# Performance work log

Hardware: AMD Instinct MI355X
Metric: run time of the kernel (lower is better)

The kernel has to match this reference:

```python
import jax, jax.numpy as jnp
import numpy as np

B, C, K, F = 16, 64, 128, 6
HORIZON_S = 3.0  # conflict_horizon_s default
EPS = 1e-06


def setup_inputs() -> dict:
    rng = np.random.default_rng(0)
    # base adjacency: sparse random directed graph, zero diagonal
    A = (rng.random((B, K, K)) < 0.05).astype(np.float32)
    A[:, np.arange(K), np.arange(K)] = 0.0
    # candidates: exactly one unordered-pair edit (state in {0:none,1:i->j,2:j->i})
    cand = np.repeat(A[:, None], C, axis=1).copy()
    i = rng.integers(0, K - 1, (B, C))
    j = i + 1 + (rng.integers(0, K - 1, (B, C)) % (K - 1 - i))
    state = rng.integers(0, 3, (B, C))
    bidx = np.arange(B)[:, None] * np.ones((1, C), dtype=np.int64)
    cidx = np.ones((B, 1), dtype=np.int64) * np.arange(C)[None, :]
    cand[bidx, cidx, i, j] = (state == 1).astype(np.float32)
    cand[bidx, cidx, j, i] = (state == 2).astype(np.float32)
    cand[:, 0] = A  # candidate 0 is NOOP (keep A_t)
    # agent features: (x, y, yaw, vx, vy, pad)
    feat = rng.normal(size=(B, K, F)).astype(np.float32)
    feat[..., 0:2] *= 20.0  # spread positions over ~40m
    mask = (rng.random((B, K)) > 0.1).astype(np.float32)
    return {
        "A_t": jnp.asarray(A),
        "candidate_A": jnp.asarray(cand),
        "agent_feat": jnp.asarray(feat),
        "agent_mask": jnp.asarray(mask),
    }


def _edit_tokens(A_t, candidate_A):
    # vectorized version of EBSTM.extract_edit_tokens
    Bn, Cn, Kn, _ = candidate_A.shape
    base = A_t > 0.5                      # [B,K,K]
    cb = candidate_A > 0.5                # [B,C,K,K]
    diff = cb != base[:, None]            # [B,C,K,K]
    upper = jnp.triu(jnp.ones((Kn, Kn), dtype=bool), k=1)
    pairdiff = (diff | jnp.swapaxes(diff, -1, -2)) & upper
    flat = pairdiff.reshape(Bn, Cn, Kn * Kn)
    changed = flat.any(-1)                # [B,C]
    idx = jnp.argmax(flat, axis=-1)       # first changed pair in row-major (i,j) order
    i = idx // Kn
    j = idx % Kn
    barange = jnp.arange(Bn)[:, None]
    carange = jnp.arange(Cn)[None, :]
    b_ij = base[barange, i, j]
    b_ji = base[barange, j, i]
    c_ij = cb[barange, carange, i, j]
    c_ji = cb[barange, carange, j, i]
    prev = jnp.where(b_ij & ~b_ji, 1, jnp.where(b_ji & ~b_ij, 2, 0))
    nxt = jnp.where(c_ij & ~c_ji, 1, jnp.where(c_ji & ~c_ij, 2, 0))
    tokens = jnp.stack([i, j, prev, nxt], axis=-1).astype(jnp.int32)
    return tokens * changed[..., None].astype(jnp.int32)


def _relation_state3(cb):
    # cb: bool [B,C,K,K]
    at = jnp.swapaxes(cb, -1, -2)
    return ((cb & ~at).astype(jnp.int32) * 1
            + (~cb & at).astype(jnp.int32) * 2
            + (cb & at).astype(jnp.int32) * 3)


def _batched_acyclic(cb, agent_mask):
    # vectorized Kahn zero-indegree peel, matching EBSTM._is_acyclic semantics:
    #  - indegree counts edges from ALL sources (valid or not)
    #  - only valid nodes are ever removed
    #  - special case: <=1 valid node is acyclic
    Bn, Cn, Kn, _ = cb.shape
    valid = (agent_mask > 0.5)[:, None, :]           # [B,1,K]
    Ai = cb.astype(jnp.int32)                        # [B,C,K,K]
    indeg = Ai.sum(axis=-2) * valid.astype(jnp.int32)  # [B,C,K]
    removed = jnp.zeros((Bn, Cn, Kn), dtype=bool)

    def body(t, carry):
        indeg, removed = carry
        rem = valid & (~removed) & (indeg == 0)
        dec = jnp.einsum('bci,bcij->bcj', rem.astype(jnp.int32), Ai)
        return indeg - dec, removed | rem

    indeg, removed = jax.lax.fori_loop(0, Kn, body, (indeg, removed))
    vcount = valid.astype(jnp.int32).sum(-1)          # [B,1]
    return (removed.astype(jnp.int32).sum(-1) == vcount) | (vcount <= 1)


def _pair_dists(agent_feat):
    pos = agent_feat[..., 0:2]
    vel = agent_feat[..., 3:5]
    # _pair_distance: d[b,i,j] = |pos_i - pos_j|
    d = jnp.linalg.norm(pos[:, :, None] - pos[:, None, :], axis=-1)
    # _pair_closest_approach_distance: r[b,i,j] = pos_j - pos_i
    r = pos[:, None, :] - pos[:, :, None]
    v = vel[:, None, :] - vel[:, :, None]
    vv = (v * v).sum(-1)
    rv = (r * v).sum(-1)
    t_star = jnp.clip(-rv / (vv + EPS), 0.0, HORIZON_S)
    dmin = jnp.linalg.norm(r + v * t_star[..., None], axis=-1)
    eye = jnp.eye(dmin.shape[-1], dtype=bool)[None]
    dmin = jnp.where(eye, jnp.inf, dmin)
    return jnp.stack([d, dmin], axis=0)  # [2,B,K,K]


def reference(A_t, candidate_A, agent_feat, agent_mask):
    cb = candidate_A > 0.5
    tokens = _edit_tokens(A_t, candidate_A)          # [B,C,4] int32
    rel = _relation_state3(cb)                       # [B,C,K,K] int32
    acyclic = _batched_acyclic(cb, agent_mask)       # [B,C] bool
    dists = _pair_dists(agent_feat)                  # [2,B,K,K] float32
    return tokens, rel, acyclic, dists
```

## Files before the change

### kernel.cpp

```cpp
#include <hip/hip_runtime.h>
#include <cstdint>
#include <math.h>

#define KN 128
#define BATCH 16
#define CAND 64

typedef float vfloat4 __attribute__((ext_vector_type(4)));

static constexpr size_t TOK_OFF = 0;
static constexpr size_t REL_OFF = (size_t)BATCH * CAND * 4;
static constexpr size_t ACY_OFF = REL_OFF + (size_t)BATCH * CAND * KN * KN;
static constexpr size_t DST_OFF = ACY_OFF + (size_t)BATCH * CAND;

#define DIAG_BIG 1.0e30f

__global__ __launch_bounds__(256) void prep_kernel(const float* __restrict__ A_t,
                                                   const float* __restrict__ feat,
                                                   uint32_t* __restrict__ bits,
                                                   float* __restrict__ out) {
    int t = threadIdx.x;
    {
        int tid  = blockIdx.x * 256 + t;
        int wave = tid >> 6;
        int lane = tid & 63;
        int half = wave & 1;
        int row  = wave >> 1;
        float v = A_t[(size_t)row * KN + half * 64 + lane];
        unsigned long long m = __ballot(v > 0.5f);
        if (lane == 0) {
            bits[row * 4 + half * 2]     = (uint32_t)m;
            bits[row * 4 + half * 2 + 1] = (uint32_t)(m >> 32);
        }
    }
    {
        int bi = 2 * blockIdx.x + (t >> 7);
        int b2 = bi >> 7, i = bi & 127, j = t & 127;
        const float* fi = feat + (size_t)bi * 6;
        const float* fj = feat + (size_t)(b2 * KN + j) * 6;
        float pix = fi[0], piy = fi[1], vix = fi[3], viy = fi[4];
        float pjx = fj[0], pjy = fj[1], vjx = fj[3], vjy = fj[4];
        float dx = pix - pjx, dy = piy - pjy;
        float d = sqrtf(dx * dx + dy * dy);
        float rx = pjx - pix, ry = pjy - piy;
        float vx = vjx - vix, vy = vjy - viy;
        float vv = vx * vx + vy * vy;
        float rv = rx * vx + ry * vy;
        float ts = fminf(fmaxf(-rv / (vv + 1e-6f), 0.0f), 3.0f);
        float mx = rx + vx * ts, my = ry + vy * ts;
        float dmin = (i == j) ? DIAG_BIG : sqrtf(mx * mx + my * my);
        float* o = out + DST_OFF;
        __builtin_nontemporal_store(d,    o + (size_t)(b2 * KN + i) * KN + j);
        __builtin_nontemporal_store(dmin, o + (size_t)((BATCH + b2) * KN + i) * KN + j);
    }
}

__global__ __launch_bounds__(256) void main_kernel(const float* __restrict__ cand,
                                                   const float* __restrict__ mask,
                                                   const uint32_t* __restrict__ baseBits,
                                                   float* __restrict__ out) {
    __shared__ uint32_t adj[KN][5];
    __shared__ uint32_t adjT[KN][6];
    __shared__ uint32_t baseB[KN][4];
    __shared__ uint32_t validW[4];
    __shared__ uint32_t remW2[2][4];
    __shared__ uint32_t removedW[4];
    __shared__ int      minIdx;

    const int t    = threadIdx.x;
    const int lane = t & 63;
    const int wave = t >> 6;
    const int bc   = blockIdx.x;
    const int b    = bc >> 6;

    const float* cptr = cand + (size_t)bc * (KN * KN);
    float* relp = out + REL_OFF + (size_t)bc * (KN * KN);

    float4 c[16];
    const int sub = lane & 31;
    #pragma unroll
    for (int m = 0; m < 16; ++m) {
        int r = (m * 4 + wave) * 2 + (lane >> 5);
        c[m] = ((const float4*)(cptr + (size_t)r * KN))[sub];
    }

    if (t == 0) minIdx = 0x7fffffff;
    if (t < 4)  removedW[t] = 0;

    for (int w = t; w < 512; w += 256) {
        baseB[w >> 2][w & 3] = baseBits[b * 512 + w];
    }

    if (wave < 2) {
        float mv = mask[b * KN + wave * 64 + lane];
        unsigned long long m = __ballot(mv > 0.5f);
        if (lane == 0) {
            validW[wave * 2]     = (uint32_t)m;
            validW[wave * 2 + 1] = (uint32_t)(m >> 32);
        }
    }

    #pragma unroll
    for (int m = 0; m < 16; ++m) {
        int r = (m * 4 + wave) * 2 + (lane >> 5);
        const float4 v = c[m];
        uint32_t nib = (v.x > 0.5f ? 1u : 0u) | (v.y > 0.5f ? 2u : 0u) |
                       (v.z > 0.5f ? 4u : 0u) | (v.w > 0.5f ? 8u : 0u);
        uint32_t word = nib << (4 * (sub & 7));
        word |= __shfl_xor(word, 1);
        word |= __shfl_xor(word, 2);
        word |= __shfl_xor(word, 4);
        if ((lane & 7) == 0) adj[r][sub >> 3] = word;
    }
    __syncthreads();

    {
        const int h = wave >> 1, q = wave & 1;
        uint32_t lo = adj[h * 64 + lane][q * 2];
        uint32_t hi = adj[h * 64 + lane][q * 2 + 1];
        unsigned long long x = ((unsigned long long)hi << 32) | lo;
        const unsigned long long Lm[6] = {
            0x5555555555555555ull, 0x3333333333333333ull, 0x0F0F0F0F0F0F0F0Full,
            0x00FF00FF00FF00FFull, 0x0000FFFF0000FFFFull, 0x00000000FFFFFFFFull };
        #pragma unroll
        for (int k = 0; k < 6; ++k) {
            const int d = 1 << k;
            const unsigned long long L = Lm[k];
            unsigned long long y = __shfl_xor((unsigned long long)x, d);
            x = (lane & d) ? ((x & ~L) | ((y & ~L) >> d))
                           : ((x & L)  | ((y & L) << d));
        }
        adjT[q * 64 + lane][2 * h]     = (uint32_t)x;
        adjT[q * 64 + lane][2 * h + 1] = (uint32_t)(x >> 32);
    }
    __syncthreads();

    uint32_t cT0 = 0, cT1 = 0, cT2 = 0, cT3 = 0;
    int  indeg = 0;
    bool validT = false;
    if (t < KN) {
        cT0 = adjT[t][0]; cT1 = adjT[t][1]; cT2 = adjT[t][2]; cT3 = adjT[t][3];
        validT = (validW[t >> 5] >> (t & 31)) & 1u;
        indeg = validT ? (__popc(cT0) + __popc(cT1) + __popc(cT2) + __popc(cT3)) : 0;
    }

    auto rel_expand = [&]() {
        #pragma unroll
        for (int m = 0; m < 16; ++m) {
            int q  = t + 256 * m;
            int i  = q >> 5;
            int j0 = (q & 31) * 4;
            int iw = j0 >> 5, sh = j0 & 31;
            uint32_t wij = adj[i][iw];
            uint32_t wti = adjT[i][iw];
            uint32_t a4 = (wij >> sh) & 0xFu;
            uint32_t b4 = (wti >> sh) & 0xFu;
            uint32_t packed = ((a4 * 0x00204081u) & 0x01010101u)
                            | (((b4 * 0x00204081u) & 0x01010101u) << 1);
            vfloat4 o;
            o.x = (float)(uint8_t)(packed);
            o.y = (float)(uint8_t)(packed >> 8);
            o.z = (float)(uint8_t)(packed >> 16);
            o.w = (float)(uint8_t)(packed >> 24);
            __builtin_nontemporal_store(o, ((vfloat4*)relp) + q);
        }
    };

    auto logic_phase = [&]() {
        for (int idx = t; idx < 512; idx += 256) {
            int i = idx >> 2, k = idx & 3;
            uint32_t diff = adj[i][k] ^ baseB[i][k];
            if (diff) {
                int base = k * 32;
                uint32_t up, low;
                if (i < base)            { up = diff; low = 0u; }
                else if (i >= base + 31) { up = 0u; low = (i > base + 31) ? diff : (diff & 0x7fffffffu); }
                else {
                    int s = i - base;
                    up  = diff & (0xffffffffu << (s + 1));
                    low = diff & ((1u << s) - 1u);
                }
                int c1 = 0x7fffffff, c2 = 0x7fffffff;
                if (up)  c1 = (i << 7) | (base + __builtin_ctz(up));
                if (low) { int cc2 = base + __builtin_ctz(low); c2 = (cc2 << 7) | i; }
                int cm = min(c1, c2);
                if (cm != 0x7fffffff) atomicMin(&minIdx, cm);
            }
        }
        __syncthreads();

        if (t == 0) {
            float* tok = out + TOK_OFF + (size_t)bc * 4;
            int mi = minIdx;
            if (mi != 0x7fffffff) {
                int i = mi >> 7, j = mi & 127;
                uint32_t b_ij = (baseB[i][j >> 5] >> (j & 31)) & 1u;
                uint32_t b_ji = (baseB[j][i >> 5] >> (i & 31)) & 1u;
                uint32_t c_ij = (adj[i][j >> 5] >> (j & 31)) & 1u;
                uint32_t c_ji = (adj[j][i >> 5] >> (i & 31)) & 1u;
                int prev = (b_ij && !b_ji) ? 1 : ((b_ji && !b_ij) ? 2 : 0);
                int nxt  = (c_ij && !c_ji) ? 1 : ((c_ji && !c_ij) ? 2 : 0);
                tok[0] = (float)i; tok[1] = (float)j; tok[2] = (float)prev; tok[3] = (float)nxt;
            } else {
                tok[0] = 0.f; tok[1] = 0.f; tok[2] = 0.f; tok[3] = 0.f;
            }
        }

        bool removed = false;
        for (int it = 0; it < KN; ++it) {
            const int bsel = it & 1;
            bool rem = (t < KN) && validT && !removed && (indeg == 0);
            unsigned long long m = __ballot(rem);
            if (wave < 2 && lane == 0) {
                remW2[bsel][wave * 2]     = (uint32_t)m;
                remW2[bsel][wave * 2 + 1] = (uint32_t)(m >> 32);
            }
            __syncthreads();
            uint32_t r0 = remW2[bsel][0], r1 = remW2[bsel][1];
            uint32_t r2 = remW2[bsel][2], r3 = remW2[bsel][3];
            if ((r0 | r1 | r2 | r3) == 0u) break;
            if (t < 4) removedW[t] |= remW2[bsel][t];
            if (t < KN) {
                indeg -= __popc(r0 & cT0) + __popc(r1 & cT1) +
                         __popc(r2 & cT2) + __popc(r3 & cT3);
                removed = removed || rem;
            }
        }
        __syncthreads();

        if (t == 0) {
            int rc = __popc(removedW[0]) + __popc(removedW[1]) + __popc(removedW[2]) + __popc(removedW[3]);
            int vc = __popc(validW[0]) + __popc(validW[1]) + __popc(validW[2]) + __popc(validW[3]);
            out[ACY_OFF + bc] = ((rc == vc) || (vc <= 1)) ? 1.0f : 0.0f;
        }
    };

    if (((bc >> 8) & 1) == 0) {
        rel_expand();
        logic_phase();
    } else {
        logic_phase();
        rel_expand();
    }
}

extern "C" void kernel_launch(void* const* d_in, const int* in_sizes, int n_in,
                              void* d_out, int out_size, void* d_ws, size_t ws_size,
                              hipStream_t stream) {
    const float* A_t  = (const float*)d_in[0];
    const float* cand = (const float*)d_in[1];
    const float* feat = (const float*)d_in[2];
    const float* mask = (const float*)d_in[3];
    float* out = (float*)d_out;
    uint32_t* bits = (uint32_t*)d_ws;

    prep_kernel<<<1024, 256, 0, stream>>>(A_t, feat, bits, out);
    main_kernel<<<BATCH * CAND, 256, 0, stream>>>(cand, mask, bits, out);
}
```

Baseline: 123.4 us.

## Split relation expansion into a separate kernel reading packed bit planes

The fused main kernel is split in two. A pack kernel reads the candidates, builds the adjacency and transpose bitsets, writes them to workspace, and computes the tokens and the acyclicity check. A separate rel kernel then expands those bit planes into the large float relation output. The aim is to separate the latency-bound Kahn loop from the bandwidth-bound relation stores so each kernel runs as a uniform phase. The cost is an extra launch and a workspace round-trip of 4 KB per candidate, and the two phases no longer overlap within one block.

Result: slower. 131.1 us (+6.2%).

```diff
diff --git a/kernel.cpp b/kernel.cpp
--- a/kernel.cpp
+++ b/kernel.cpp
@@ -14,6 +14,9 @@
 static constexpr size_t DST_OFF = ACY_OFF + (size_t)BATCH * CAND;
 
 #define DIAG_BIG 1.0e30f
+
+static constexpr size_t WS_BITS  = 0;
+static constexpr size_t WS_PLANE = 2048;
 
 __global__ __launch_bounds__(256) void prep_kernel(const float* __restrict__ A_t,
                                                    const float* __restrict__ feat,
@@ -55,9 +58,10 @@
     }
 }
 
-__global__ __launch_bounds__(256) void main_kernel(const float* __restrict__ cand,
+__global__ __launch_bounds__(256) void pack_kernel(const float* __restrict__ cand,
                                                    const float* __restrict__ mask,
                                                    const uint32_t* __restrict__ baseBits,
+                                                   uint32_t* __restrict__ planes,
                                                    float* __restrict__ out) {
     __shared__ uint32_t adj[KN][5];
     __shared__ uint32_t adjT[KN][6];
@@ -74,7 +78,6 @@
     const int b    = bc >> 6;
 
     const float* cptr = cand + (size_t)bc * (KN * KN);
-    float* relp = out + REL_OFF + (size_t)bc * (KN * KN);
 
     float4 c[16];
     const int sub = lane & 31;
@@ -135,6 +138,55 @@
     }
     __syncthreads();
 
+    {
+        uint32_t* pb = planes + (size_t)bc * 1024;
+        #pragma unroll
+        for (int rep = 0; rep < 2; ++rep) {
+            int w = t + rep * 256;
+            pb[w]       = adj[w >> 2][w & 3];
+            pb[512 + w] = adjT[w >> 2][w & 3];
+        }
+    }
+
+    for (int idx = t; idx < 512; idx += 256) {
+        int i = idx >> 2, k = idx & 3;
+        uint32_t diff = adj[i][k] ^ baseB[i][k];
+        if (diff) {
+            int base = k * 32;
+            uint32_t up, low;
+            if (i < base)            { up = diff; low = 0u; }
+            else if (i >= base + 31) { up = 0u; low = (i > base + 31) ? diff : (diff & 0x7fffffffu); }
+            else {
+                int s = i - base;
+                up  = diff & (0xffffffffu << (s + 1));
+                low = diff & ((1u << s) - 1u);
+            }
+            int c1 = 0x7fffffff, c2 = 0x7fffffff;
+            if (up)  c1 = (i << 7) | (base + __builtin_ctz(up));
+            if (low) { int cc2 = base + __builtin_ctz(low); c2 = (cc2 << 7) | i; }
+            int cm = min(c1, c2);
+            if (cm != 0x7fffffff) atomicMin(&minIdx, cm);
+        }
+    }
+    __syncthreads();
+
+    if (t == 0) {
+        float* tok = out + TOK_OFF + (size_t)bc * 4;
+        int mi = minIdx;
+        if (mi != 0x7fffffff) {
+            int i = mi >> 7, j = mi & 127;
+            uint32_t b_ij = (baseB[i][j >> 5] >> (j & 31)) & 1u;
+            uint32_t b_ji = (baseB[j][i >> 5] >> (i & 31)) & 1u;
+            uint32_t c_ij = (adj[i][j >> 5] >> (j & 31)) & 1u;
+            uint32_t c_ji = (adj[j][i >> 5] >> (i & 31)) & 1u;
+            int prev = (b_ij && !b_ji) ? 1 : ((b_ji && !b_ij) ? 2 : 0);
+            int nxt  = (c_ij && !c_ji) ? 1 : ((c_ji && !c_ij) ? 2 : 0);
+            tok[0] = (float)i; tok[1] = (float)j; tok[2] = (float)prev; tok[3] = (float)nxt;
+        } else {
+            tok[0] = 0.f; tok[1] = 0.f; tok[2] = 0.f; tok[3] = 0.f;
+        }
+    }
+
     uint32_t cT0 = 0, cT1 = 0, cT2 = 0, cT3 = 0;
     int  indeg = 0;
     bool validT = false;
@@ -144,103 +196,65 @@
         indeg = validT ? (__popc(cT0) + __popc(cT1) + __popc(cT2) + __popc(cT3)) : 0;
     }
 
-    auto rel_expand = [&]() {
-        #pragma unroll
-        for (int m = 0; m < 16; ++m) {
-            int q  = t + 256 * m;
-            int i  = q >> 5;
-            int j0 = (q & 31) * 4;
-            int iw = j0 >> 5, sh = j0 & 31;
-            uint32_t wij = adj[i][iw];
-            uint32_t wti = adjT[i][iw];
-            uint32_t a4 = (wij >> sh) & 0xFu;
-            uint32_t b4 = (wti >> sh) & 0xFu;
-            uint32_t packed = ((a4 * 0x00204081u) & 0x01010101u)
-                            | (((b4 * 0x00204081u) & 0x01010101u) << 1);
-            vfloat4 o;
-            o.x = (float)(uint8_t)(packed);
-            o.y = (float)(uint8_t)(packed >> 8);
-            o.z = (float)(uint8_t)(packed >> 16);
-            o.w = (float)(uint8_t)(packed >> 24);
-            __builtin_nontemporal_store(o, ((vfloat4*)relp) + q);
-        }
-    };
-
-    auto logic_phase = [&]() {
-        for (int idx = t; idx < 512; idx += 256) {
-            int i = idx >> 2, k = idx & 3;
-            uint32_t diff = adj[i][k] ^ baseB[i][k];
-            if (diff) {
-                int base = k * 32;
-                uint32_t up, low;
-                if (i < base)            { up = diff; low = 0u; }
-                else if (i >= base + 31) { up = 0u; low = (i > base + 31) ? diff : (diff & 0x7fffffffu); }
-                else {
-                    int s = i - base;
-                    up  = diff & (0xffffffffu << (s + 1));
-                    low = diff & ((1u << s) - 1u);
-                }
-                int c1 = 0x7fffffff, c2 = 0x7fffffff;
-                if (up)  c1 = (i << 7) | (base + __builtin_ctz(up));
-                if (low) { int cc2 = base + __builtin_ctz(low); c2 = (cc2 << 7) | i; }
-                int cm = min(c1, c2);
-                if (cm != 0x7fffffff) atomicMin(&minIdx, cm);
-            }
+    bool removed = false;
+    for (int it = 0; it < KN; ++it) {
+        const int bsel = it & 1;
+        bool rem = (t < KN) && validT && !removed && (indeg == 0);
+        unsigned long long m = __ballot(rem);
+        if (wave < 2 && lane == 0) {
+            remW2[bsel][wave * 2]     = (uint32_t)m;
+            remW2[bsel][wave * 2 + 1] = (uint32_t)(m >> 32);
         }
         __syncthreads();
-
-        if (t == 0) {
-            float* tok = out + TOK_OFF + (size_t)bc * 4;
-            int mi = minIdx;
-            if (mi != 0x7fffffff) {
-                int i = mi >> 7, j = mi & 127;
-                uint32_t b_ij = (baseB[i][j >> 5] >> (j & 31)) & 1u;
-                uint32_t b_ji = (baseB[j][i >> 5] >> (i & 31)) & 1u;
-                uint32_t c_ij = (adj[i][j >> 5] >> (j & 31)) & 1u;
-                uint32_t c_ji = (adj[j][i >> 5] >> (i & 31)) & 1u;
-                int prev = (b_ij && !b_ji) ? 1 : ((b_ji && !b_ij) ? 2 : 0);
-                int nxt  = (c_ij && !c_ji) ? 1 : ((c_ji && !c_ij) ? 2 : 0);
-                tok[0] = (float)i; tok[1] = (float)j; tok[2] = (float)prev; tok[3] = (float)nxt;
-            } else {
-                tok[0] = 0.f; tok[1] = 0.f; tok[2] = 0.f; tok[3] = 0.f;
-            }
-        }
-
-        bool removed = false;
-        for (int it = 0; it < KN; ++it) {
-            const int bsel = it & 1;
-            bool rem = (t < KN) && validT && !removed && (indeg == 0);
-            unsigned long long m = __ballot(rem);
-            if (wave < 2 && lane == 0) {
-                remW2[bsel][wave * 2]     = (uint32_t)m;
-                remW2[bsel][wave * 2 + 1] = (uint32_t)(m >> 32);
-            }
-            __syncthreads();
-            uint32_t r0 = remW2[bsel][0], r1 = remW2[bsel][1];
-            uint32_t r2 = remW2[bsel][2], r3 = remW2[bsel][3];
-            if ((r0 | r1 | r2 | r3) == 0u) break;
-            if (t < 4) removedW[t] |= remW2[bsel][t];
-            if (t < KN) {
-                indeg -= __popc(r0 & cT0) + __popc(r1 & cT1) +
-                         __popc(r2 & cT2) + __popc(r3 & cT3);
-                removed = removed || rem;
-            }
-        }
-        __syncthreads();
-
-        if (t == 0) {
-            int rc = __popc(removedW[0]) + __popc(removedW[1]) + __popc(removedW[2]) + __popc(removedW[3]);
-            int vc = __popc(validW[0]) + __popc(validW[1]) + __popc(validW[2]) + __popc(validW[3]);
-            out[ACY_OFF + bc] = ((rc == vc) || (vc <= 1)) ? 1.0f : 0.0f;
-        }
-    };
-
-    if (((bc >> 8) & 1) == 0) {
-        rel_expand();
-        logic_phase();
-    } else {
-        logic_phase();
-        rel_expand();
+        uint32_t r0 = remW2[bsel][0], r1 = remW2[bsel][1];
+        uint32_t r2 = remW2[bsel][2], r3 = remW2[bsel][3];
+        if ((r0 | r1 | r2 | r3) == 0u) break;
+        if (t < 4) removedW[t] |= remW2[bsel][t];
+        if (t < KN) {
+            indeg -= __popc(r0 & cT0) + __popc(r1 & cT1) +
+                     __popc(r2 & cT2) + __popc(r3 & cT3);
+            removed = removed || rem;
+        }
+    }
+    __syncthreads();
+
+    if (t == 0) {
+        int rc = __popc(removedW[0]) + __popc(removedW[1]) + __popc(removedW[2]) + __popc(removedW[3]);
+        int vc = __popc(validW[0]) + __popc(validW[1]) + __popc(validW[2]) + __popc(validW[3]);
+        out[ACY_OFF + bc] = ((rc == vc) || (vc <= 1)) ? 1.0f : 0.0f;
+    }
+}
+
+__global__ __launch_bounds__(256) void rel_kernel(const uint32_t* __restrict__ planes,
+                                                  float* __restrict__ out) {
+    __shared__ uint32_t plane[1024];
+
+    const int t  = threadIdx.x;
+    const int bc = blockIdx.x;
+
+    uint4 v = ((const uint4*)(planes + (size_t)bc * 1024))[t];
+    ((uint4*)plane)[t] = v;
+    __syncthreads();
+
+    float* relp = out + REL_OFF + (size_t)bc * (KN * KN);
+    #pragma unroll
+    for (int m = 0; m < 16; ++m) {
+        int q  = t + 256 * m;
+        int i  = q >> 5;
+        int j0 = (q & 31) * 4;
+        int iw = j0 >> 5, sh = j0 & 31;
+        uint32_t wij = plane[i * 4 + iw];
+        uint32_t wti = plane[512 + i * 4 + iw];
+        uint32_t a4 = (wij >> sh) & 0xFu;
+        uint32_t b4 = (wti >> sh) & 0xFu;
+        uint32_t packed = ((a4 * 0x00204081u) & 0x01010101u)
+                        | (((b4 * 0x00204081u) & 0x01010101u) << 1);
+        vfloat4 o;
+        o.x = (float)(uint8_t)(packed);
+        o.y = (float)(uint8_t)(packed >> 8);
+        o.z = (float)(uint8_t)(packed >> 16);
+        o.w = (float)(uint8_t)(packed >> 24);
+        __builtin_nontemporal_store(o, ((vfloat4*)relp) + q);
     }
 }
 
@@ -252,8 +266,11 @@
     const float* feat = (const float*)d_in[2];
     const float* mask = (const float*)d_in[3];
     float* out = (float*)d_out;
-    uint32_t* bits = (uint32_t*)d_ws;
+    uint32_t* ws   = (uint32_t*)d_ws;
+    uint32_t* bits   = ws + WS_BITS;
+    uint32_t* planes = ws + WS_PLANE;
 
     prep_kernel<<<1024, 256, 0, stream>>>(A_t, feat, bits, out);
-    main_kernel<<<BATCH * CAND, 256, 0, stream>>>(cand, mask, bits, out);
-}
+    pack_kernel<<<BATCH * CAND, 256, 0, stream>>>(cand, mask, bits, planes, out);
+    rel_kernel<<<BATCH * CAND, 256, 0, stream>>>(planes, out);
+}
```
